# Performance work log

Measured on AMD Instinct MI355X. Metric: run time of the kernel, lower is better.

## Reference

```python
import jax, jax.numpy as jnp
import numpy as np


def setup_inputs() -> dict:
    key = jax.random.key(0)
    ks = jax.random.split(key, 7)
    OUT, IN, K = 4096, 4096, 2048
    U_STORED, VT_STORED = 512, 1024  # int(0.5*(K//2+1)), int(0.5*(IN//2+1))
    return {
        "x": jax.random.normal(ks[0], (1024, IN), dtype=jnp.float32),
        "U_real": jax.random.normal(ks[1], (OUT, U_STORED), dtype=jnp.float32) * 0.01,
        "U_imag": jax.random.normal(ks[2], (OUT, U_STORED), dtype=jnp.float32) * 0.01,
        "S": jax.random.normal(ks[3], (K,), dtype=jnp.float32) * 0.02,
        "Vt_real": jax.random.normal(ks[4], (K, VT_STORED), dtype=jnp.float32) * 0.01,
        "Vt_imag": jax.random.normal(ks[5], (K, VT_STORED), dtype=jnp.float32) * 0.01,
        "bias": jnp.zeros((OUT,), dtype=jnp.float32),
    }


def _decompress(coeffs_real, coeffs_imag, n):
    # Zero-pad truncated rfft coefficients back to n//2+1, then inverse rfft.
    c = jax.lax.complex(coeffs_real, coeffs_imag)
    num_unique = n // 2 + 1
    pad = num_unique - c.shape[-1]
    if pad > 0:
        c = jnp.pad(c, ((0, 0), (0, pad)))
    elif pad < 0:
        c = c[..., :num_unique]
    return jnp.fft.irfft(c, n=n, axis=-1)


def reference(x, U_real, U_imag, S, Vt_real, Vt_imag, bias):
    k_rank = S.shape[0]
    in_features = x.shape[-1]
    U = _decompress(U_real, U_imag, k_rank)            # (out, k)
    Vh = _decompress(Vt_real, Vt_imag, in_features)    # (k, in)
    W = (U * S[None, :]) @ Vh                          # (out, in) reconstructed weight
    return x @ W.T + bias                              # F.linear(x, W, bias)
```

## Files before the change

kernel.cpp:

```cpp
#include <hip/hip_runtime.h>
#include <math.h>
#include <stdint.h>

#define PI2 6.28318530717958647692f

typedef __bf16 bf16x8 __attribute__((ext_vector_type(8)));
typedef float f32x4 __attribute__((ext_vector_type(4)));

typedef __attribute__((address_space(1))) const void gvoid_t;
typedef __attribute__((address_space(3))) void lvoid_t;

__device__ __forceinline__ void g2l16(const void* g, void* l) {
    __builtin_amdgcn_global_load_lds(
        reinterpret_cast<gvoid_t*>(reinterpret_cast<uintptr_t>(g)),
        reinterpret_cast<lvoid_t*>(reinterpret_cast<uintptr_t>(l)),
        16, 0, 0);
}

__device__ __forceinline__ short f2bf(float f) {
    unsigned u = __float_as_uint(f);
    u += 0x7FFFu + ((u >> 16) & 1u);
    return (short)(u >> 16);
}

__device__ __forceinline__ unsigned pack2bf(float a, float b) {
    return (unsigned)(unsigned short)f2bf(a) |
           ((unsigned)(unsigned short)f2bf(b) << 16);
}

__device__ __forceinline__ float bflo(unsigned v) { return __uint_as_float(v << 16); }
__device__ __forceinline__ float bfhi(unsigned v) { return __uint_as_float(v & 0xFFFF0000u); }

__device__ __forceinline__ int xcd_swizzle(int blk, int G) {
    return (blk & 7) * (G >> 3) + (blk >> 3);
}

__global__ __launch_bounds__(256) void aux_all8(
    const float* __restrict__ x,
    const float* __restrict__ Ur, const float* __restrict__ Ui,
    const float* __restrict__ S,
    const float* __restrict__ Vr, const float* __restrict__ Vi,
    short* __restrict__ xe, short* __restrict__ xo,
    short* __restrict__ B1f, short* __restrict__ Vcat,
    short* __restrict__ B2, short* __restrict__ Ucat)
{
    unsigned i8 = (blockIdx.x * 256u + threadIdx.x) * 8u;
    if (i8 < 2097152u) {
        unsigned i = i8;
        int r = i >> 11, j0 = i & 2047;
        const float* xr = x + (size_t)r * 4096 + j0;
        float4 a0 = ((const float4*)xr)[0], a1 = ((const float4*)xr)[1];
        float4 b0 = ((const float4*)(xr + 2048))[0],
               b1 = ((const float4*)(xr + 2048))[1];
        uint4 oe = {pack2bf(a0.x + b0.x, a0.y + b0.y),
                    pack2bf(a0.z + b0.z, a0.w + b0.w),
                    pack2bf(a1.x + b1.x, a1.y + b1.y),
                    pack2bf(a1.z + b1.z, a1.w + b1.w)};
        *(uint4*)(xe + i) = oe;
        uint4 oo = {pack2bf(a0.x - b0.x, a0.y - b0.y),
                    pack2bf(a0.z - b0.z, a0.w - b0.w),
                    pack2bf(a1.x - b1.x, a1.y - b1.y),
                    pack2bf(a1.z - b1.z, a1.w - b1.w)};
        *(uint4*)(xo + i) = oo;
    } else if (i8 < 6291456u) {
        unsigned i = i8 - 2097152u;
        int r = i >> 11, j0 = i & 2047;
        const float inv_n = 1.0f / 4096.0f;
        float v[8];
        if (r < 512) {
            if (r == 0) {
                #pragma unroll
                for (int u = 0; u < 8; ++u) v[u] = inv_n;
            } else {
                #pragma unroll
                for (int u = 0; u < 8; ++u) {
                    int t = (r * (j0 + u)) & 2047;
                    v[u] = 2.0f * inv_n * cosf((float)t * (PI2 / 2048.0f));
                }
            }
        } else if (r < 1024) {
            int m = r - 512;
            #pragma unroll
            for (int u = 0; u < 8; ++u) {
                int t = (m * (j0 + u)) & 2047;
                v[u] = -2.0f * inv_n * sinf((float)t * (PI2 / 2048.0f));
            }
        } else if (r < 1536) {
            int c = 2 * (r - 1024) + 1;
            #pragma unroll
            for (int u = 0; u < 8; ++u) {
                int t = (c * (j0 + u)) & 4095;
                v[u] = 2.0f * inv_n * cosf((float)t * (PI2 / 4096.0f));
            }
        } else {
            int m = 2 * (r - 1536) + 1;
            #pragma unroll
            for (int u = 0; u < 8; ++u) {
                int t = (m * (j0 + u)) & 4095;
                v[u] = -2.0f * inv_n * sinf((float)t * (PI2 / 4096.0f));
            }
        }
        uint4 o = {pack2bf(v[0], v[1]), pack2bf(v[2], v[3]),
                   pack2bf(v[4], v[5]), pack2bf(v[6], v[7])};
        *(uint4*)(B1f + i) = o;
    } else if (i8 < 10485760u) {
        unsigned i = i8 - 6291456u;
        int k = i >> 11, c0 = i & 2047;
        int cls = c0 >> 9, cc0 = c0 & 511;
        const float* src = ((cls & 1) ? Vi : Vr) + (size_t)k * 1024 + 2 * cc0;
        float4 q0 = ((const float4*)src)[0];
        float4 q1 = ((const float4*)src)[1];
        float4 q2 = ((const float4*)src)[2];
        float4 q3 = ((const float4*)src)[3];
        float v[8];
        if ((cls >> 1) == 0) {
            v[0] = q0.x; v[1] = q0.z; v[2] = q1.x; v[3] = q1.z;
            v[4] = q2.x; v[5] = q2.z; v[6] = q3.x; v[7] = q3.z;
        } else {
            v[0] = q0.y; v[1] = q0.w; v[2] = q1.y; v[3] = q1.w;
            v[4] = q2.y; v[5] = q2.w; v[6] = q3.y; v[7] = q3.w;
        }
        uint4 o = {pack2bf(v[0], v[1]), pack2bf(v[2], v[3]),
                   pack2bf(v[4], v[5]), pack2bf(v[6], v[7])};
        *(uint4*)(Vcat + i) = o;
    } else if (i8 < 12582912u) {
        unsigned i = i8 - 10485760u;
        int p = i >> 11, k0 = i & 2047;
        float4 s0 = *(const float4*)(S + k0);
        float4 s1 = *(const float4*)(S + k0 + 4);
        float sv[8] = {s0.x, s0.y, s0.z, s0.w, s1.x, s1.y, s1.z, s1.w};
        const float inv_n = 1.0f / 2048.0f;
        float v[8];
        if (p == 0) {
            #pragma unroll
            for (int u = 0; u < 8; ++u) v[u] = inv_n * sv[u];
        } else if (p < 512) {
            #pragma unroll
            for (int u = 0; u < 8; ++u) {
                int t = (p * (k0 + u)) & 2047;
                v[u] = 2.0f * inv_n * cosf((float)t * (PI2 / 2048.0f)) * sv[u];
            }
        } else {
            int q = p - 512;
            #pragma unroll
            for (int u = 0; u < 8; ++u) {
                int t = (q * (k0 + u)) & 2047;
                v[u] = -2.0f * inv_n * sinf((float)t * (PI2 / 2048.0f)) * sv[u];
            }
        }
        uint4 o = {pack2bf(v[0], v[1]), pack2bf(v[2], v[3]),
                   pack2bf(v[4], v[5]), pack2bf(v[6], v[7])};
        *(uint4*)(B2 + i) = o;
    } else {
        unsigned i = i8 - 12582912u;
        int o_ = i >> 10, c = i & 1023;
        const float* src = (c < 512) ? (Ur + (size_t)o_ * 512 + c)
                                     : (Ui + (size_t)o_ * 512 + (c - 512));
        float4 a = ((const float4*)src)[0], b = ((const float4*)src)[1];
        uint4 o = {pack2bf(a.x, a.y), pack2bf(a.z, a.w),
                   pack2bf(b.x, b.y), pack2bf(b.z, b.w)};
        *(uint4*)(Ucat + i) = o;
    }
}

__device__ __forceinline__ void tile_core(
    const short* __restrict__ A, int lda,
    const short* __restrict__ B, int ldb, int K,
    short* As, short* Bs, int bm, int bn, f32x4 (&acc)[4][4])
{
    const int tid  = threadIdx.x;
    const int wave = tid >> 6;
    const int lane = tid & 63;
    const int wm   = (wave >> 1) << 6;
    const int wn   = (wave & 1) << 6;
    const int l16  = lane & 15;
    const int quad = lane >> 4;
    const int rk   = l16 & 7;

    int aoff[4], boff[4], loff[4];
    #pragma unroll
    for (int p = 0; p < 4; ++p) {
        int L   = p * 256 + wave * 64 + lane;
        int row = L >> 3;
        int swz = (L & 7) ^ (row & 7);
        aoff[p] = (bm + row) * lda + swz * 8;
        boff[p] = (bn + row) * ldb + swz * 8;
        loff[p] = L * 8;
    }

    for (int k0 = 0; k0 < K; k0 += 64) {
        __syncthreads();
        #pragma unroll
        for (int p = 0; p < 4; ++p) g2l16(A + aoff[p] + k0, As + loff[p]);
        #pragma unroll
        for (int p = 0; p < 4; ++p) g2l16(B + boff[p] + k0, Bs + loff[p]);
        __syncthreads();

        #pragma unroll
        for (int h = 0; h < 2; ++h) {
            const int cs8 = ((((h << 2) | quad) ^ rk) << 3);
            bf16x8 b[4];
            #pragma unroll
            for (int nt = 0; nt < 4; ++nt)
                b[nt] = *(const bf16x8*)(Bs + (wn + nt * 16 + l16) * 64 + cs8);
            #pragma unroll
            for (int mt = 0; mt < 4; ++mt) {
                bf16x8 a = *(const bf16x8*)(As + (wm + mt * 16 + l16) * 64 + cs8);
                #pragma unroll
                for (int nt = 0; nt < 4; ++nt)
                    acc[mt][nt] = __builtin_amdgcn_mfma_f32_16x16x32_bf16(
                        a, b[nt], acc[mt][nt], 0, 0, 0);
            }
        }
    }
}

__device__ __forceinline__ void store_tile_bf16(
    f32x4 (&acc)[4][4], short* __restrict__ C, int ldc, int bm, int bn)
{
    const int tid  = threadIdx.x;
    const int wave = tid >> 6;
    const int lane = tid & 63;
    const int wm   = (wave >> 1) << 6;
    const int wn   = (wave & 1) << 6;
    const int l16  = lane & 15;
    const int quad = lane >> 4;
    #pragma unroll
    for (int nt = 0; nt < 4; ++nt) {
        int col = bn + wn + nt * 16 + l16;
        #pragma unroll
        for (int mt = 0; mt < 4; ++mt) {
            int rowb = bm + wm + mt * 16 + quad * 4;
            #pragma unroll
            for (int r = 0; r < 4; ++r)
                C[(size_t)(rowb + r) * ldc + col] = f2bf(acc[mt][nt][r]);
        }
    }
}

__device__ __forceinline__ void store_frag(
    f32x4 (&acc)[4][4], short* __restrict__ planeTile)
{
    uint4* p = (uint4*)planeTile;
    const int tid = threadIdx.x;
    #pragma unroll
    for (int c = 0; c < 8; ++c) {
        int nt = c >> 1, mt0 = (c & 1) * 2;
        uint4 o = {pack2bf(acc[mt0][nt][0],     acc[mt0][nt][1]),
                   pack2bf(acc[mt0][nt][2],     acc[mt0][nt][3]),
                   pack2bf(acc[mt0 + 1][nt][0], acc[mt0 + 1][nt][1]),
                   pack2bf(acc[mt0 + 1][nt][2], acc[mt0 + 1][nt][3])};
        p[c * 256 + tid] = o;
    }
}

template <bool OUT_F32>
__device__ __forceinline__ void reduce_unit(
    const short* __restrict__ P, size_t planeU4, int SK,
    int tile, int c, int tilesX, void* __restrict__ Out, int ldc,
    const float* __restrict__ bias)
{
    const int bm = (tile / tilesX) << 7;
    const int bn = (tile % tilesX) << 7;
    const int tid  = threadIdx.x;
    const int wave = tid >> 6;
    const int lane = tid & 63;
    const int wm   = (wave >> 1) << 6;
    const int wn   = (wave & 1) << 6;
    const int l16  = lane & 15;
    const int quad = lane >> 4;
    const int nt   = c >> 1, mt0 = (c & 1) * 2;

    const uint4* P4 = (const uint4*)P;
    const size_t base = (size_t)tile * 2048 + (size_t)c * 256 + tid;
    float f[8] = {0, 0, 0, 0, 0, 0, 0, 0};
    for (int z = 0; z < SK; ++z) {
        uint4 v = P4[(size_t)z * planeU4 + base];
        f[0] += bflo(v.x); f[1] += bfhi(v.x);
        f[2] += bflo(v.y); f[3] += bfhi(v.y);
        f[4] += bflo(v.z); f[5] += bfhi(v.z);
        f[6] += bflo(v.w); f[7] += bfhi(v.w);
    }
    const int col = bn + wn + nt * 16 + l16;
    float bv = 0.f;
    if (OUT_F32) bv = bias[col];
    #pragma unroll
    for (int j = 0; j < 8; ++j) {
        int mt  = mt0 + (j >> 2);
        int row = bm + wm + mt * 16 + quad * 4 + (j & 3);
        if (OUT_F32)
            ((float*)Out)[(size_t)row * ldc + col] = f[j] + bv;
        else
            ((short*)Out)[(size_t)row * ldc + col] = f2bf(f[j]);
    }
}

__global__ __launch_bounds__(256, 4) void gemm_s1f(
    const short* __restrict__ xe, const short* __restrict__ xo,
    const short* __restrict__ B1f, short* __restrict__ P)
{
    __shared__ __align__(16) short As[128 * 64];
    __shared__ __align__(16) short Bs[128 * 64];

    f32x4 acc[4][4];
    #pragma unroll
    for (int i = 0; i < 4; ++i)
        #pragma unroll
        for (int j = 0; j < 4; ++j)
            acc[i][j] = (f32x4){0.f, 0.f, 0.f, 0.f};

    const int u    = xcd_swizzle((int)blockIdx.x, (int)gridDim.x);
    const int z    = u >> 7;
    const int tile = u & 127;
    const int tx   = tile & 15, ty = tile >> 4;
    const bool odd = (tx & 8) != 0;
    const short* A = (odd ? xo : xe) + (size_t)z * 256;
    const short* B = B1f + (odd ? (size_t)1024 * 2048 : 0) + (size_t)z * 256;
    const int bm   = ty << 7;
    const int bn   = (tx & 7) << 7;

    tile_core(A, 2048, B, 2048, 256, As, Bs, bm, bn, acc);
    store_frag(acc, P + (size_t)z * 2097152 + (size_t)tile * 16384);
}

__global__ __launch_bounds__(256, 4) void gemm_sk_frag(
    const short* __restrict__ A, int lda,
    const short* __restrict__ B, int ldb,
    short* __restrict__ P, size_t planeShorts, int Kpart,
    int tileShift, int tilesXShift)
{
    __shared__ __align__(16) short As[128 * 64];
    __shared__ __align__(16) short Bs[128 * 64];

    f32x4 acc[4][4];
    #pragma unroll
    for (int i = 0; i < 4; ++i)
        #pragma unroll
        for (int j = 0; j < 4; ++j)
            acc[i][j] = (f32x4){0.f, 0.f, 0.f, 0.f};

    const int u    = xcd_swizzle((int)blockIdx.x, (int)gridDim.x);
    const int z    = u >> tileShift;
    const int tile = u & ((1 << tileShift) - 1);
    const int bm   = (tile >> tilesXShift) << 7;
    const int bn   = (tile & ((1 << tilesXShift) - 1)) << 7;

    tile_core(A + (size_t)z * Kpart, lda, B + (size_t)z * Kpart, ldb, Kpart,
              As, Bs, bm, bn, acc);
    store_frag(acc, P + (size_t)z * planeShorts + (size_t)tile * 16384);
}

template <bool OUT_F32>
__global__ __launch_bounds__(256) void reduce_frag(
    const short* __restrict__ P, size_t planeShorts, int SK,
    int tilesX, void* __restrict__ Out, int ldc,
    const float* __restrict__ bias)
{
    reduce_unit<OUT_F32>(P, planeShorts >> 3, SK,
                         (int)(blockIdx.x >> 3), (int)(blockIdx.x & 7),
                         tilesX, Out, ldc, bias);
}

template <bool OUT_F32>
__global__ __launch_bounds__(256, 4) void gemm_direct(
    const short* __restrict__ A, int lda,
    const short* __restrict__ B, int ldb,
    void* __restrict__ Cv, int ldc,
    const float* __restrict__ bias, int K)
{
    __shared__ __align__(16) short As[128 * 64];
    __shared__ __align__(16) short Bs[128 * 64];

    f32x4 acc[4][4];
    #pragma unroll
    for (int i = 0; i < 4; ++i)
        #pragma unroll
        for (int j = 0; j < 4; ++j)
            acc[i][j] = (f32x4){0.f, 0.f, 0.f, 0.f};

    const int bm = blockIdx.y << 7;
    const int bn = blockIdx.x << 7;
    tile_core(A, lda, B, ldb, K, As, Bs, bm, bn, acc);

    const int tid  = threadIdx.x;
    const int wave = tid >> 6;
    const int lane = tid & 63;
    const int wm   = (wave >> 1) << 6;
    const int wn   = (wave & 1) << 6;
    const int l16  = lane & 15;
    const int quad = lane >> 4;

    if (OUT_F32) {
        float* C = (float*)Cv;
        #pragma unroll
        for (int nt = 0; nt < 4; ++nt) {
            int col = bn + wn + nt * 16 + l16;
            float bv = bias ? bias[col] : 0.f;
            #pragma unroll
            for (int mt = 0; mt < 4; ++mt) {
                int rowb = bm + wm + mt * 16 + quad * 4;
                #pragma unroll
                for (int r = 0; r < 4; ++r)
                    C[(size_t)(rowb + r) * ldc + col] = acc[mt][nt][r] + bv;
            }
        }
    } else {
        store_tile_bf16(acc, (short*)Cv, ldc, bm, bn);
    }
}

extern "C" void kernel_launch(void* const* d_in, const int* in_sizes, int n_in,
                              void* d_out, int out_size, void* d_ws, size_t ws_size,
                              hipStream_t stream) {
    const float* x    = (const float*)d_in[0];
    const float* Ur   = (const float*)d_in[1];
    const float* Ui   = (const float*)d_in[2];
    const float* S    = (const float*)d_in[3];
    const float* Vr   = (const float*)d_in[4];
    const float* Vi   = (const float*)d_in[5];
    const float* bias = (const float*)d_in[6];
    float* out = (float*)d_out;

    short* ws   = (short*)d_ws;
    short* xe   = ws;
    short* xo   = xe   + (size_t)1024 * 2048;
    short* B1f  = xo   + (size_t)1024 * 2048;
    short* Vcat = B1f  + (size_t)2048 * 2048;
    short* B2   = Vcat + (size_t)2048 * 2048;
    short* Ucat = B2   + (size_t)1024 * 2048;
    short* Xp   = Ucat + (size_t)4096 * 1024;
    short* T1   = Xp   + (size_t)1024 * 2048;
    short* Gm   = T1   + (size_t)1024 * 2048;
    short* Pp   = Gm   + (size_t)1024 * 1024;

    const size_t need = (size_t)((char*)(Pp + (size_t)16777216) - (char*)d_ws);

    aux_all8<<<dim3(8192), 256, 0, stream>>>(
        x, Ur, Ui, S, Vr, Vi, xe, xo, B1f, Vcat, B2, Ucat);

    if (ws_size >= need) {
        gemm_s1f<<<dim3(1024), 256, 0, stream>>>(xe, xo, B1f, Pp);
        reduce_frag<false><<<dim3(1024), 256, 0, stream>>>(
            Pp, (size_t)2097152, 8, 16, Xp, 2048, nullptr);

        gemm_sk_frag<<<dim3(1024), 256, 0, stream>>>(
            Xp, 2048, Vcat, 2048, Pp, (size_t)2097152, 256, 7, 4);
        reduce_frag<false><<<dim3(1024), 256, 0, stream>>>(
            Pp, (size_t)2097152, 8, 16, T1, 2048, nullptr);

        gemm_sk_frag<<<dim3(512), 256, 0, stream>>>(
            T1, 2048, B2, 2048, Pp, (size_t)1048576, 256, 6, 3);
        reduce_frag<false><<<dim3(512), 256, 0, stream>>>(
            Pp, (size_t)1048576, 8, 8, Gm, 1024, nullptr);

        gemm_sk_frag<<<dim3(1024), 256, 0, stream>>>(
            Gm, 1024, Ucat, 1024, Pp, (size_t)4194304, 256, 8, 5);
        reduce_frag<true><<<dim3(2048), 256, 0, stream>>>(
            Pp, (size_t)4194304, 4, 32, out, 4096, bias);
    } else {
        gemm_direct<false><<<dim3(8, 8), 256, 0, stream>>>(
            xe, 2048, B1f, 2048, Xp, 2048, nullptr, 2048);
        gemm_direct<false><<<dim3(8, 8), 256, 0, stream>>>(
            xo, 2048, B1f + (size_t)1024 * 2048, 2048, Xp + 1024, 2048,
            nullptr, 2048);
        gemm_direct<false><<<dim3(16, 8), 256, 0, stream>>>(
            Xp, 2048, Vcat, 2048, T1, 2048, nullptr, 2048);
        gemm_direct<false><<<dim3(8, 8), 256, 0, stream>>>(
            T1, 2048, B2, 2048, Gm, 1024, nullptr, 2048);
        gemm_direct<true><<<dim3(32, 8), 256, 0, stream>>>(
            Gm, 1024, Ucat, 1024, out, 4096, bias, 1024);
    }
}
```

Measured before the change: 191.3 us.

## Fuse split-K reductions into GEMM kernels via atomic tile counters

Removes the four separate reduce_frag launches. Each split-K GEMM block now bumps an atomic per-tile counter after storing its partial, and the last block to arrive sums all partials and writes the output tile. The counters are zeroed by an extra block appended to the aux kernel. Split-K factors are also lowered (8→4, 8→4, 4→2 for three stages), which halves the grids to 512 blocks and reduces partial-buffer traffic. The cost is less parallelism per stage and a serialized reduction tail handled by the last block of each tile.

Measured after the change: 395.0 us. 106% more time.

```diff
diff --git a/kernel.cpp b/kernel.cpp
--- a/kernel.cpp
+++ b/kernel.cpp
@@ -42,8 +42,15 @@
     const float* __restrict__ Vr, const float* __restrict__ Vi,
     short* __restrict__ xe, short* __restrict__ xo,
     short* __restrict__ B1f, short* __restrict__ Vcat,
-    short* __restrict__ B2, short* __restrict__ Ucat)
-{
+    short* __restrict__ B2, short* __restrict__ Ucat,
+    int* __restrict__ cnt)
+{
+    if (blockIdx.x >= 8192) {
+        if (cnt) {
+            for (int t = threadIdx.x; t < 576; t += 256) cnt[t] = 0;
+        }
+        return;
+    }
     unsigned i8 = (blockIdx.x * 256u + threadIdx.x) * 8u;
     if (i8 < 2097152u) {
         unsigned i = i8;
@@ -255,13 +262,13 @@
 }
 
 template <bool OUT_F32>
-__device__ __forceinline__ void reduce_unit(
+__device__ __forceinline__ void reduce_tile(
     const short* __restrict__ P, size_t planeU4, int SK,
-    int tile, int c, int tilesX, void* __restrict__ Out, int ldc,
+    int tile, int tilesXShift, void* __restrict__ Out, int ldc,
     const float* __restrict__ bias)
 {
-    const int bm = (tile / tilesX) << 7;
-    const int bn = (tile % tilesX) << 7;
+    const int bm = (tile >> tilesXShift) << 7;
+    const int bn = (tile & ((1 << tilesXShift) - 1)) << 7;
     const int tid  = threadIdx.x;
     const int wave = tid >> 6;
     const int lane = tid & 63;
@@ -269,35 +276,60 @@
     const int wn   = (wave & 1) << 6;
     const int l16  = lane & 15;
     const int quad = lane >> 4;
-    const int nt   = c >> 1, mt0 = (c & 1) * 2;
 
     const uint4* P4 = (const uint4*)P;
-    const size_t base = (size_t)tile * 2048 + (size_t)c * 256 + tid;
-    float f[8] = {0, 0, 0, 0, 0, 0, 0, 0};
-    for (int z = 0; z < SK; ++z) {
-        uint4 v = P4[(size_t)z * planeU4 + base];
-        f[0] += bflo(v.x); f[1] += bfhi(v.x);
-        f[2] += bflo(v.y); f[3] += bfhi(v.y);
-        f[4] += bflo(v.z); f[5] += bfhi(v.z);
-        f[6] += bflo(v.w); f[7] += bfhi(v.w);
-    }
-    const int col = bn + wn + nt * 16 + l16;
-    float bv = 0.f;
-    if (OUT_F32) bv = bias[col];
-    #pragma unroll
-    for (int j = 0; j < 8; ++j) {
-        int mt  = mt0 + (j >> 2);
-        int row = bm + wm + mt * 16 + quad * 4 + (j & 3);
-        if (OUT_F32)
-            ((float*)Out)[(size_t)row * ldc + col] = f[j] + bv;
-        else
-            ((short*)Out)[(size_t)row * ldc + col] = f2bf(f[j]);
-    }
-}
-
-__global__ __launch_bounds__(256, 4) void gemm_s1f(
+    #pragma unroll
+    for (int c = 0; c < 8; ++c) {
+        const int nt = c >> 1, mt0 = (c & 1) * 2;
+        const size_t base = (size_t)tile * 2048 + (size_t)c * 256 + tid;
+        float f[8] = {0, 0, 0, 0, 0, 0, 0, 0};
+        for (int z = 0; z < SK; ++z) {
+            uint4 v = P4[(size_t)z * planeU4 + base];
+            f[0] += bflo(v.x); f[1] += bfhi(v.x);
+            f[2] += bflo(v.y); f[3] += bfhi(v.y);
+            f[4] += bflo(v.z); f[5] += bfhi(v.z);
+            f[6] += bflo(v.w); f[7] += bfhi(v.w);
+        }
+        const int col = bn + wn + nt * 16 + l16;
+        float bv = 0.f;
+        if (OUT_F32) bv = bias[col];
+        #pragma unroll
+        for (int j = 0; j < 8; ++j) {
+            int mt  = mt0 + (j >> 2);
+            int row = bm + wm + mt * 16 + quad * 4 + (j & 3);
+            if (OUT_F32)
+                ((float*)Out)[(size_t)row * ldc + col] = f[j] + bv;
+            else
+                ((short*)Out)[(size_t)row * ldc + col] = f2bf(f[j]);
+        }
+    }
+}
+
+template <bool OUT_F32>
+__device__ __forceinline__ void sk_finish(
+    const short* __restrict__ P, size_t planeShorts, int SK,
+    int tile, int tilesXShift, int* __restrict__ cnt,
+    void* __restrict__ Out, int ldc, const float* __restrict__ bias)
+{
+    __shared__ int s_old;
+    __syncthreads();
+    if (threadIdx.x == 0) {
+        __threadfence();
+        s_old = __hip_atomic_fetch_add(cnt + tile, 1,
+                                       __ATOMIC_ACQ_REL, __HIP_MEMORY_SCOPE_AGENT);
+    }
+    __syncthreads();
+    if (s_old == SK - 1) {
+        __threadfence();
+        reduce_tile<OUT_F32>(P, planeShorts >> 3, SK, tile, tilesXShift,
+                             Out, ldc, bias);
+    }
+}
+
+__global__ __launch_bounds__(256, 4) void gemm_s1f_fused(
     const short* __restrict__ xe, const short* __restrict__ xo,
-    const short* __restrict__ B1f, short* __restrict__ P)
+    const short* __restrict__ B1f, short* __restrict__ P,
+    int* __restrict__ cnt, short* __restrict__ Xp)
 {
     __shared__ __align__(16) short As[128 * 64];
     __shared__ __align__(16) short Bs[128 * 64];
@@ -314,20 +346,24 @@
     const int tile = u & 127;
     const int tx   = tile & 15, ty = tile >> 4;
     const bool odd = (tx & 8) != 0;
-    const short* A = (odd ? xo : xe) + (size_t)z * 256;
-    const short* B = B1f + (odd ? (size_t)1024 * 2048 : 0) + (size_t)z * 256;
+    const short* A = (odd ? xo : xe) + (size_t)z * 512;
+    const short* B = B1f + (odd ? (size_t)1024 * 2048 : 0) + (size_t)z * 512;
     const int bm   = ty << 7;
     const int bn   = (tx & 7) << 7;
 
-    tile_core(A, 2048, B, 2048, 256, As, Bs, bm, bn, acc);
+    tile_core(A, 2048, B, 2048, 512, As, Bs, bm, bn, acc);
     store_frag(acc, P + (size_t)z * 2097152 + (size_t)tile * 16384);
-}
-
-__global__ __launch_bounds__(256, 4) void gemm_sk_frag(
+    sk_finish<false>(P, (size_t)2097152, 4, tile, 4, cnt, Xp, 2048, nullptr);
+}
+
+template <bool OUT_F32>
+__global__ __launch_bounds__(256, 4) void gemm_sk_fused(
     const short* __restrict__ A, int lda,
     const short* __restrict__ B, int ldb,
     short* __restrict__ P, size_t planeShorts, int Kpart,
-    int tileShift, int tilesXShift)
+    int tileShift, int tilesXShift, int SK,
+    int* __restrict__ cnt, void* __restrict__ Out, int ldc,
+    const float* __restrict__ bias)
 {
     __shared__ __align__(16) short As[128 * 64];
     __shared__ __align__(16) short Bs[128 * 64];
@@ -348,17 +384,8 @@
     tile_core(A + (size_t)z * Kpart, lda, B + (size_t)z * Kpart, ldb, Kpart,
               As, Bs, bm, bn, acc);
     store_frag(acc, P + (size_t)z * planeShorts + (size_t)tile * 16384);
-}
-
-template <bool OUT_F32>
-__global__ __launch_bounds__(256) void reduce_frag(
-    const short* __restrict__ P, size_t planeShorts, int SK,
-    int tilesX, void* __restrict__ Out, int ldc,
-    const float* __restrict__ bias)
-{
-    reduce_unit<OUT_F32>(P, planeShorts >> 3, SK,
-                         (int)(blockIdx.x >> 3), (int)(blockIdx.x & 7),
-                         tilesX, Out, ldc, bias);
+    sk_finish<OUT_F32>(P, planeShorts, SK, tile, tilesXShift, cnt,
+                       Out, ldc, bias);
 }
 
 template <bool OUT_F32>
@@ -432,31 +459,30 @@
     short* T1   = Xp   + (size_t)1024 * 2048;
     short* Gm   = T1   + (size_t)1024 * 2048;
     short* Pp   = Gm   + (size_t)1024 * 1024;
-
-    const size_t need = (size_t)((char*)(Pp + (size_t)16777216) - (char*)d_ws);
-
-    aux_all8<<<dim3(8192), 256, 0, stream>>>(
-        x, Ur, Ui, S, Vr, Vi, xe, xo, B1f, Vcat, B2, Ucat);
-
-    if (ws_size >= need) {
-        gemm_s1f<<<dim3(1024), 256, 0, stream>>>(xe, xo, B1f, Pp);
-        reduce_frag<false><<<dim3(1024), 256, 0, stream>>>(
-            Pp, (size_t)2097152, 8, 16, Xp, 2048, nullptr);
-
-        gemm_sk_frag<<<dim3(1024), 256, 0, stream>>>(
-            Xp, 2048, Vcat, 2048, Pp, (size_t)2097152, 256, 7, 4);
-        reduce_frag<false><<<dim3(1024), 256, 0, stream>>>(
-            Pp, (size_t)2097152, 8, 16, T1, 2048, nullptr);
-
-        gemm_sk_frag<<<dim3(512), 256, 0, stream>>>(
-            T1, 2048, B2, 2048, Pp, (size_t)1048576, 256, 6, 3);
-        reduce_frag<false><<<dim3(512), 256, 0, stream>>>(
-            Pp, (size_t)1048576, 8, 8, Gm, 1024, nullptr);
-
-        gemm_sk_frag<<<dim3(1024), 256, 0, stream>>>(
-            Gm, 1024, Ucat, 1024, Pp, (size_t)4194304, 256, 8, 5);
-        reduce_frag<true><<<dim3(2048), 256, 0, stream>>>(
-            Pp, (size_t)4194304, 4, 32, out, 4096, bias);
+    int*   cnt  = (int*)(Pp + (size_t)8388608);
+
+    const size_t need = (size_t)((char*)(cnt + 576) - (char*)d_ws);
+    const bool   big  = (ws_size >= need);
+
+    aux_all8<<<dim3(8193), 256, 0, stream>>>(
+        x, Ur, Ui, S, Vr, Vi, xe, xo, B1f, Vcat, B2, Ucat,
+        big ? cnt : nullptr);
+
+    if (big) {
+        gemm_s1f_fused<<<dim3(512), 256, 0, stream>>>(
+            xe, xo, B1f, Pp, cnt, Xp);
+
+        gemm_sk_fused<false><<<dim3(512), 256, 0, stream>>>(
+            Xp, 2048, Vcat, 2048, Pp, (size_t)2097152, 512, 7, 4, 4,
+            cnt + 128, T1, 2048, nullptr);
+
+        gemm_sk_fused<false><<<dim3(512), 256, 0, stream>>>(
+            T1, 2048, B2, 2048, Pp, (size_t)1048576, 256, 6, 3, 8,
+            cnt + 256, Gm, 1024, nullptr);
+
+        gemm_sk_fused<true><<<dim3(512), 256, 0, stream>>>(
+            Gm, 1024, Ucat, 1024, Pp, (size_t)4194304, 512, 8, 5, 2,
+            cnt + 320, out, 4096, bias);
     } else {
         gemm_direct<false><<<dim3(8, 8), 256, 0, stream>>>(
             xe, 2048, B1f, 2048, Xp, 2048, nullptr, 2048);
```
